# Performance work log

Hardware: AMD Instinct MI355X
Metric: run time of the kernel (lower is better)

## Reference

```python
import jax, jax.numpy as jnp
import numpy as np

D = 768
H = 12
DH = D // H
PAIRS4 = [(0, 1), (0, 2), (0, 3), (1, 2), (1, 3), (2, 3)]
J6 = jnp.array([[0,0,0,0,0,1],[0,0,0,0,-1,0],[0,0,0,1,0,0],[0,0,1,0,0,0],[0,-1,0,0,0,0],[1,0,0,0,0,0]], dtype=jnp.float32)


def exterior(p1, p2):
    # p1,p2: (..., 4) -> normalized Plucker coords (..., 6)
    parts = [p1[..., i] * p2[..., j] - p1[..., j] * p2[..., i] for i, j in PAIRS4]
    L = jnp.stack(parts, axis=-1)
    n = jnp.clip(jnp.linalg.norm(L, axis=-1, keepdims=True), 1e-12)
    return L / n


def layernorm(x, g, b, eps=1e-5):
    m = jnp.mean(x, axis=-1, keepdims=True)
    v = jnp.var(x, axis=-1, keepdims=True)
    return (x - m) * jax.lax.rsqrt(v + eps) * g + b


def setup_inputs() -> dict:
    key = jax.random.key(0)
    ks = jax.random.split(key, 16)
    s = 0.02
    inp = {
        'x': jax.random.normal(ks[0], (1, 2048, D), dtype=jnp.float32),
        'ln1_g': jnp.ones((D,), jnp.float32), 'ln1_b': jnp.zeros((D,), jnp.float32),
        'qkv_w': jax.random.normal(ks[1], (D, 3 * D), jnp.float32) * s,
        'qkv_b': jnp.zeros((3 * D,), jnp.float32),
        'w1_write': jax.random.normal(ks[2], (D, 4 * H), jnp.float32) * s,
        'w2_write': jax.random.normal(ks[3], (D, 4 * H), jnp.float32) * s,
        'w1_read': jax.random.normal(ks[4], (D, 4 * H), jnp.float32) * s,
        'w2_read': jax.random.normal(ks[5], (D, 4 * H), jnp.float32) * s,
        'geo_v_w': jax.random.normal(ks[6], (D, D), jnp.float32) * s,
        'geo_v_b': jnp.zeros((D,), jnp.float32),
        'gate_w': jax.random.normal(ks[7], (D, H), jnp.float32) * s,
        'gate_b': jnp.zeros((H,), jnp.float32),
        'inc_scale': jnp.ones((H,), jnp.float32),
        'out_w': jax.random.normal(ks[8], (D, D), jnp.float32) * s,
        'out_b': jnp.zeros((D,), jnp.float32),
        'ln2_g': jnp.ones((D,), jnp.float32), 'ln2_b': jnp.zeros((D,), jnp.float32),
        'fc_w': jax.random.normal(ks[9], (D, 4 * D), jnp.float32) * s,
        'fc_b': jnp.zeros((4 * D,), jnp.float32),
        'proj_w': jax.random.normal(ks[10], (4 * D, D), jnp.float32) * s,
        'proj_b': jnp.zeros((D,), jnp.float32),
    }
    return inp


def dual_path_attention(x, qkv_w, qkv_b, w1_write, w2_write, w1_read, w2_read,
                        geo_v_w, geo_v_b, gate_w, gate_b, inc_scale, out_w, out_b):
    B, T, _ = x.shape
    scale = DH ** -0.5
    qkv = (x @ qkv_w + qkv_b).reshape(B, T, 3, H, DH)
    q = qkv[:, :, 0].transpose(0, 2, 1, 3)  # (B,H,T,dh)
    k = qkv[:, :, 1].transpose(0, 2, 1, 3)
    v = qkv[:, :, 2].transpose(0, 2, 1, 3)
    std_logits = jnp.einsum('bhtd,bhsd->bhts', q, k) * scale

    x_prev = jnp.concatenate([jnp.zeros((B, 1, x.shape[-1]), x.dtype), x[:, :-1]], axis=1)
    w1 = (x_prev @ w1_write).reshape(B, T, H, 4)
    w2 = (x @ w2_write).reshape(B, T, H, 4)
    write_lines = exterior(w1, w2)  # (B,T,H,6)
    r1 = (x @ w1_read).reshape(B, T, H, 4)
    r2 = (x @ w2_read).reshape(B, T, H, 4)
    read_lines = exterior(r1, r2)
    J_write = jnp.einsum('bthi,ij->bthj', write_lines, J6)
    geo_logits = jnp.einsum('bthp,bshp->bhts', read_lines, J_write)
    geo_logits = geo_logits * inc_scale[None, :, None, None]

    mask = jnp.triu(jnp.ones((T, T), dtype=bool), k=1)  # True above diagonal
    neg = jnp.finfo(x.dtype).min
    std_attn = jax.nn.softmax(jnp.where(mask, neg, std_logits), axis=-1)
    std_out = jnp.einsum('bhts,bhsd->bthd', std_attn, v).reshape(B, T, -1)
    geo_attn = jax.nn.softmax(jnp.where(mask, neg, geo_logits), axis=-1)
    geo_v = (x @ geo_v_w + geo_v_b).reshape(B, T, H, DH).transpose(0, 2, 1, 3)
    geo_out = jnp.einsum('bhts,bhsd->bthd', geo_attn, geo_v).reshape(B, T, -1)

    gate = jax.nn.sigmoid(x @ gate_w + gate_b).mean(axis=-1, keepdims=True)
    combined = (1 - gate) * std_out + gate * geo_out
    return combined @ out_w + out_b


def reference(x, ln1_g, ln1_b, qkv_w, qkv_b, w1_write, w2_write, w1_read, w2_read,
              geo_v_w, geo_v_b, gate_w, gate_b, inc_scale, out_w, out_b,
              ln2_g, ln2_b, fc_w, fc_b, proj_w, proj_b):
    h = x + dual_path_attention(layernorm(x, ln1_g, ln1_b), qkv_w, qkv_b,
                                w1_write, w2_write, w1_read, w2_read,
                                geo_v_w, geo_v_b, gate_w, gate_b, inc_scale,
                                out_w, out_b)
    m = layernorm(h, ln2_g, ln2_b)
    mlp = jax.nn.gelu(m @ fc_w + fc_b) @ proj_w + proj_b
    return h + mlp
```

## Files before the change

### kernel.cpp

```cpp
#include <hip/hip_runtime.h>
#include <hip/hip_bf16.h>
#include <math.h>

#define TT 2048
#define DD 768

typedef __bf16 bf16x8 __attribute__((ext_vector_type(8)));
typedef float f32x4 __attribute__((ext_vector_type(4)));

__device__ __forceinline__ void gload16(const void* g, void* l) {
    __builtin_amdgcn_global_load_lds(
        (const __attribute__((address_space(1))) unsigned int*)g,
        (__attribute__((address_space(3))) unsigned int*)l, 16, 0, 0);
}

__device__ __forceinline__ bf16x8 zero8() {
    bf16x8 v;
    #pragma unroll
    for (int j = 0; j < 8; ++j) v[j] = (__bf16)0.0f;
    return v;
}

__global__ __launch_bounds__(256) void ln_kernel(const float* __restrict__ in,
    const float* __restrict__ g, const float* __restrict__ b,
    __hip_bfloat16* __restrict__ out)
{
    const int t = blockIdx.x;
    const int tid = threadIdx.x;
    const float* row = in + (size_t)t * DD;
    float x0 = row[tid], x1 = row[tid + 256], x2 = row[tid + 512];
    float s = x0 + x1 + x2;
    float q = x0 * x0 + x1 * x1 + x2 * x2;
    #pragma unroll
    for (int m = 1; m < 64; m <<= 1) {
        s += __shfl_xor(s, m);
        q += __shfl_xor(q, m);
    }
    __shared__ float ssum[4], sqsum[4];
    const int w = tid >> 6;
    if ((tid & 63) == 0) { ssum[w] = s; sqsum[w] = q; }
    __syncthreads();
    s = ssum[0] + ssum[1] + ssum[2] + ssum[3];
    q = sqsum[0] + sqsum[1] + sqsum[2] + sqsum[3];
    const float mean = s * (1.0f / DD);
    const float var = q * (1.0f / DD) - mean * mean;
    const float rs = rsqrtf(var + 1e-5f);
    __hip_bfloat16* orow = out + (size_t)t * DD;
    orow[tid]       = __float2bfloat16((x0 - mean) * rs * g[tid]       + b[tid]);
    orow[tid + 256] = __float2bfloat16((x1 - mean) * rs * g[tid + 256] + b[tid + 256]);
    orow[tid + 512] = __float2bfloat16((x2 - mean) * rs * g[tid + 512] + b[tid + 512]);
}

__global__ __launch_bounds__(256) void castT_kernel(const float* __restrict__ in,
    __hip_bfloat16* __restrict__ out, int K, int N)
{
    __shared__ float t[32][33];
    const int n0 = blockIdx.x << 5, k0 = blockIdx.y << 5;
    const int tx = threadIdx.x & 31, ty = threadIdx.x >> 5;
    #pragma unroll
    for (int i = 0; i < 32; i += 8)
        t[ty + i][tx] = in[(size_t)(k0 + ty + i) * N + n0 + tx];
    __syncthreads();
    #pragma unroll
    for (int i = 0; i < 32; i += 8)
        out[(size_t)(n0 + ty + i) * K + k0 + tx] = __float2bfloat16(t[tx][ty + i]);
}

__global__ __launch_bounds__(256) void wcat_kernel(
    const float* __restrict__ w2w, const float* __restrict__ w1w,
    const float* __restrict__ w1r, const float* __restrict__ w2r,
    const float* __restrict__ gw, __hip_bfloat16* __restrict__ Wcat)
{
    const int nrow = blockIdx.x;
    const float* src; int col, stride;
    if (nrow < 48)       { src = w2w; col = nrow;       stride = 48; }
    else if (nrow < 96)  { src = w1w; col = nrow - 48;  stride = 48; }
    else if (nrow < 144) { src = w1r; col = nrow - 96;  stride = 48; }
    else if (nrow < 192) { src = w2r; col = nrow - 144; stride = 48; }
    else                 { src = gw;  col = nrow - 192; stride = 12; }
    const int tid = threadIdx.x;
    #pragma unroll
    for (int i = 0; i < 3; ++i) {
        const int k = tid + (i << 8);
        Wcat[(size_t)nrow * 768 + k] = __float2bfloat16(src[(size_t)k * stride + col]);
    }
}

__device__ __forceinline__ float gelu_f(float x) {
    float u = 0.7978845608028654f * (x + 0.044715f * x * x * x);
    return 0.5f * x * (1.0f + tanhf(u));
}

__global__ __launch_bounds__(256) void mgemm64_kernel(
    const __hip_bfloat16* __restrict__ A, const __hip_bfloat16* __restrict__ Bt,
    const float* __restrict__ bias, const float* __restrict__ resid,
    void* __restrict__ Cout, float* __restrict__ Pb0, float* __restrict__ Pb1,
    int M, int N, int K, int kz, int epi, int omode)
{
    __shared__ __hip_bfloat16 As[64 * 32];
    __shared__ __hip_bfloat16 Bs[128 * 32];
    const int tid = threadIdx.x;
    const int lane = tid & 63, w = tid >> 6;
    const int colBase = blockIdx.x << 7, rowBase = blockIdx.y << 6;
    const int z = blockIdx.z;
    const int Kc = K / kz, koff = z * Kc;

    const int lr = lane >> 2, pc = lane & 3;
    const int n = lane & 15, quad = lane >> 4;

    const int arow = (w << 4) + lr;
    const int ac = (pc ^ ((arow >> 1) & 3)) << 3;
    const int brow0 = (w << 5) + lr, brow1 = brow0 + 16;
    const int bc0 = (pc ^ ((brow0 >> 1) & 3)) << 3;
    const int bc1 = (pc ^ ((brow1 >> 1) & 3)) << 3;

    f32x4 acc[8];
    #pragma unroll
    for (int j = 0; j < 8; ++j) acc[j] = (f32x4){0.f, 0.f, 0.f, 0.f};

    const int arF = (w << 4) + n;
    const int aposF = (quad ^ ((arF >> 1) & 3)) << 3;

    for (int kk = koff; kk < koff + Kc; kk += 32) {
        __syncthreads();
        gload16(A  + (size_t)(rowBase + arow) * K + kk + ac,   &As[(w << 4) * 32]);
        gload16(Bt + (size_t)(colBase + brow0) * K + kk + bc0, &Bs[(w << 5) * 32]);
        gload16(Bt + (size_t)(colBase + brow1) * K + kk + bc1, &Bs[((w << 5) + 16) * 32]);
        __syncthreads();

        bf16x8 af = *(const bf16x8*)&As[arF * 32 + aposF];
        #pragma unroll
        for (int j = 0; j < 8; ++j) {
            const int rb = (j << 4) + n;
            bf16x8 bfj = *(const bf16x8*)&Bs[rb * 32 + ((quad ^ ((rb >> 1) & 3)) << 3)];
            acc[j] = __builtin_amdgcn_mfma_f32_16x16x32_bf16(af, bfj, acc[j], 0, 0, 0);
        }
    }

    if (kz == 1) {
        #pragma unroll
        for (int j = 0; j < 8; ++j) {
            const int col = colBase + (j << 4) + n;
            const float bj = bias ? bias[col] : 0.f;
            #pragma unroll
            for (int r = 0; r < 4; ++r) {
                const int row = rowBase + (w << 4) + (quad << 2) + r;
                float v = acc[j][r] + bj;
                if (epi == 1) v = gelu_f(v);
                else if (epi == 2) v += resid[(size_t)row * N + col];
                if (omode == 1) ((__hip_bfloat16*)Cout)[(size_t)row * N + col] = __float2bfloat16(v);
                else ((float*)Cout)[(size_t)row * N + col] = v;
            }
        }
    } else {
        float* P = (z == 0) ? Pb0 : Pb1;
        #pragma unroll
        for (int j = 0; j < 8; ++j) {
            const int col = colBase + (j << 4) + n;
            #pragma unroll
            for (int r = 0; r < 4; ++r) {
                const int row = rowBase + (w << 4) + (quad << 2) + r;
                P[(size_t)row * N + col] = acc[j][r];
            }
        }
    }
}

__global__ __launch_bounds__(256) void kred_kernel(
    const float* __restrict__ p0, const float* __restrict__ p1,
    const float* __restrict__ bias, const float* __restrict__ resid,
    float* __restrict__ out, int N)
{
    const int base = (blockIdx.x * 256 + threadIdx.x) << 2;
    float4 a = *(const float4*)&p0[base];
    float4 b = *(const float4*)&p1[base];
    float4 bi = *(const float4*)&bias[base % N];
    float4 rs = *(const float4*)&resid[base];
    float4 o;
    o.x = a.x + b.x + bi.x + rs.x;
    o.y = a.y + b.y + bi.y + rs.y;
    o.z = a.z + b.z + bi.z + rs.z;
    o.w = a.w + b.w + bi.w + rs.w;
    *(float4*)&out[base] = o;
}

__device__ __forceinline__ void exterior6(const float* a, const float* b, float* L) {
    L[0] = a[0] * b[1] - a[1] * b[0];
    L[1] = a[0] * b[2] - a[2] * b[0];
    L[2] = a[0] * b[3] - a[3] * b[0];
    L[3] = a[1] * b[2] - a[2] * b[1];
    L[4] = a[1] * b[3] - a[3] * b[1];
    L[5] = a[2] * b[3] - a[3] * b[2];
    float n = sqrtf(L[0]*L[0] + L[1]*L[1] + L[2]*L[2] + L[3]*L[3] + L[4]*L[4] + L[5]*L[5]);
    float inv = 1.f / fmaxf(n, 1e-12f);
    #pragma unroll
    for (int p = 0; p < 6; ++p) L[p] *= inv;
}

__global__ __launch_bounds__(64) void extgate_kernel(
    const float* __restrict__ P, const float* __restrict__ gb,
    __hip_bfloat16* __restrict__ rlb, __hip_bfloat16* __restrict__ jwb,
    float* __restrict__ gate)
{
    const int t = blockIdx.x;
    const int tid = threadIdx.x;
    const float* row = P + (size_t)t * 256;
    if (tid < 12) {
        const int h = tid;
        float a[4], b[4], L[6];
        #pragma unroll
        for (int i = 0; i < 4; ++i) {
            a[i] = (t > 0) ? row[-256 + 48 + h * 4 + i] : 0.f;
            b[i] = row[h * 4 + i];
        }
        exterior6(a, b, L);
        __hip_bfloat16* jwp = jwb + (size_t)h * 16384 + t * 8;
        jwp[0] = __float2bfloat16( L[5]); jwp[1] = __float2bfloat16(-L[4]);
        jwp[2] = __float2bfloat16( L[3]); jwp[3] = __float2bfloat16( L[2]);
        jwp[4] = __float2bfloat16(-L[1]); jwp[5] = __float2bfloat16( L[0]);
        jwp[6] = __float2bfloat16(0.f);   jwp[7] = __float2bfloat16(0.f);
        #pragma unroll
        for (int i = 0; i < 4; ++i) { a[i] = row[96 + h * 4 + i]; b[i] = row[144 + h * 4 + i]; }
        exterior6(a, b, L);
        __hip_bfloat16* rlp = rlb + (size_t)h * 16384 + t * 8;
        #pragma unroll
        for (int p = 0; p < 6; ++p) rlp[p] = __float2bfloat16(L[p]);
        rlp[6] = __float2bfloat16(0.f); rlp[7] = __float2bfloat16(0.f);
    }
    if (tid == 32) {
        float g = 0.f;
        #pragma unroll
        for (int i = 0; i < 12; ++i) g += 1.f / (1.f + __expf(-(row[192 + i] + gb[i])));
        gate[t] = g * (1.f / 12.f);
    }
}

__global__ __launch_bounds__(256) void vt_kernel(
    const __hip_bfloat16* __restrict__ qkvB, const __hip_bfloat16* __restrict__ geovB,
    __hip_bfloat16* __restrict__ VT, __hip_bfloat16* __restrict__ GVT)
{
    __shared__ __hip_bfloat16 tile[64][72];
    const int s0 = blockIdx.x << 6, h = blockIdx.y;
    const bool isGV = (blockIdx.z != 0);
    const __hip_bfloat16* src = isGV ? (geovB + h * 64) : (qkvB + 1536 + h * 64);
    const int stride = isGV ? 768 : 2304;
    __hip_bfloat16* dst = (isGV ? GVT : VT) + (size_t)h * 131072;
    const int tid = threadIdx.x;
    const int r = tid >> 2, c = (tid & 3) << 3;
    *(bf16x8*)&tile[r][c]      = *(const bf16x8*)&src[(size_t)(s0 + r) * stride + c];
    *(bf16x8*)&tile[r][c + 32] = *(const bf16x8*)&src[(size_t)(s0 + r) * stride + c + 32];
    __syncthreads();
    __hip_bfloat16 tmp[8];
    #pragma unroll
    for (int j = 0; j < 8; ++j) tmp[j] = tile[c + j][r];
    *(bf16x8*)&dst[(size_t)r * 2048 + s0 + c] = *(const bf16x8*)tmp;
    #pragma unroll
    for (int j = 0; j < 8; ++j) tmp[j] = tile[c + 32 + j][r];
    *(bf16x8*)&dst[(size_t)r * 2048 + s0 + c + 32] = *(const bf16x8*)tmp;
}

__global__ __launch_bounds__(256) void mattn_kernel(
    const __hip_bfloat16* __restrict__ qkvB, const __hip_bfloat16* __restrict__ VT,
    const __hip_bfloat16* __restrict__ GVT, const __hip_bfloat16* __restrict__ rlb,
    const __hip_bfloat16* __restrict__ jwb, const float* __restrict__ gate,
    const float* __restrict__ inc_scale, __hip_bfloat16* __restrict__ comb,
    __hip_bfloat16* __restrict__ Opart, float* __restrict__ stats)
{
    __shared__ __hip_bfloat16 Ks0[2048], Ks1[2048];
    __shared__ __hip_bfloat16 VTs0[2048], VTs1[2048];
    __shared__ __hip_bfloat16 GVTs0[2048], GVTs1[2048];
    __shared__ __hip_bfloat16 JWs[64][8];
    __shared__ __bf16 Ps[64][72];
    __shared__ __bf16 Pg[64][72];

    const int j = 59 - blockIdx.x;
    const int hh = blockIdx.y;
    int qt, c, nc;
    if (j < 12)      { qt = j; c = 0; nc = 1; }
    else if (j < 36) { int t2 = j - 12; qt = 12 + (t2 >> 1); c = t2 & 1; nc = 2; }
    else             { int t2 = j - 36; int d3 = t2 / 3; qt = 24 + d3; c = t2 - d3 * 3; nc = 3; }
    const int q0 = qt << 6;
    const int nk = qt + 1;
    const int ktb = c * nk / nc;
    const int kte = (c + 1) * nk / nc - 1;
    const int tid = threadIdx.x;
    const int w = tid >> 6, lane = tid & 63;
    const int n = lane & 15, quad = lane >> 4;

    const int qrow = q0 + (w << 4) + n;
    const size_t qb = (size_t)qrow * 2304 + hh * 64;
    bf16x8 af0 = *(const bf16x8*)&qkvB[qb + (quad << 3)];
    bf16x8 af1 = *(const bf16x8*)&qkvB[qb + 32 + (quad << 3)];
    bf16x8 rlA = zero8();
    if (quad == 0) rlA = *(const bf16x8*)&rlb[(size_t)hh * 16384 + (size_t)qrow * 8];
    const float isc = inc_scale[hh];
    const float mgc = fabsf(isc);
    const size_t vbase = (size_t)hh * 131072;

    const int sRow = tid >> 2, sc = tid & 3;
    const int sPos = ((sc ^ ((sRow >> 1) & 3)) << 3);
    const int sOff = sc << 3;

    f32x4 Os[4], Og[4];
    float m_s[4], lsp[4], lgp[4];
    #pragma unroll
    for (int r = 0; r < 4; ++r) {
        m_s[r] = -1e30f; lsp[r] = 0.f; lgp[r] = 0.f;
        Os[r] = (f32x4){0.f, 0.f, 0.f, 0.f};
        Og[r] = (f32x4){0.f, 0.f, 0.f, 0.f};
    }

    bf16x8 rK0, rK1, rV0, rV1, rG0, rG1, rJ = zero8();
    {
        const int k0 = ktb << 6;
        const size_t kb = (size_t)(k0 + sRow) * 2304 + 768 + hh * 64;
        const size_t vb = vbase + (size_t)sRow * 2048 + k0;
        rK0 = *(const bf16x8*)&qkvB[kb + sOff];
        rK1 = *(const bf16x8*)&qkvB[kb + sOff + 32];
        rV0 = *(const bf16x8*)&VT[vb + sOff];
        rV1 = *(const bf16x8*)&VT[vb + sOff + 32];
        rG0 = *(const bf16x8*)&GVT[vb + sOff];
        rG1 = *(const bf16x8*)&GVT[vb + sOff + 32];
        if (tid < 64) rJ = *(const bf16x8*)&jwb[(size_t)hh * 16384 + (size_t)(k0 + tid) * 8];
    }

    for (int kt = ktb; kt <= kte; ++kt) {
        const int k0 = kt << 6;
        __syncthreads();
        *(bf16x8*)&Ks0[sRow * 32 + sPos]  = rK0;
        *(bf16x8*)&Ks1[sRow * 32 + sPos]  = rK1;
        *(bf16x8*)&VTs0[sRow * 32 + sPos] = rV0;
        *(bf16x8*)&VTs1[sRow * 32 + sPos] = rV1;
        *(bf16x8*)&GVTs0[sRow * 32 + sPos] = rG0;
        *(bf16x8*)&GVTs1[sRow * 32 + sPos] = rG1;
        if (tid < 64) *(bf16x8*)&JWs[tid][0] = rJ;
        if (kt < kte) {
            const int k1 = (kt + 1) << 6;
            const size_t kb = (size_t)(k1 + sRow) * 2304 + 768 + hh * 64;
            const size_t vb = vbase + (size_t)sRow * 2048 + k1;
            rK0 = *(const bf16x8*)&qkvB[kb + sOff];
            rK1 = *(const bf16x8*)&qkvB[kb + sOff + 32];
            rV0 = *(const bf16x8*)&VT[vb + sOff];
            rV1 = *(const bf16x8*)&VT[vb + sOff + 32];
            rG0 = *(const bf16x8*)&GVT[vb + sOff];
            rG1 = *(const bf16x8*)&GVT[vb + sOff + 32];
            if (tid < 64) rJ = *(const bf16x8*)&jwb[(size_t)hh * 16384 + (size_t)(k1 + tid) * 8];
        }
        __syncthreads();

        f32x4 Ss[4], Sg[4];
        #pragma unroll
        for (int t = 0; t < 4; ++t) {
            Ss[t] = (f32x4){0.f, 0.f, 0.f, 0.f};
            Sg[t] = (f32x4){0.f, 0.f, 0.f, 0.f};
        }
        #pragma unroll
        for (int t = 0; t < 4; ++t) {
            const int krow = (t << 4) + n;
            const int kpos = ((quad ^ ((krow >> 1) & 3)) << 3);
            bf16x8 kb0 = *(const bf16x8*)&Ks0[krow * 32 + kpos];
            bf16x8 kb1 = *(const bf16x8*)&Ks1[krow * 32 + kpos];
            Ss[t] = __builtin_amdgcn_mfma_f32_16x16x32_bf16(af0, kb0, Ss[t], 0, 0, 0);
            Ss[t] = __builtin_amdgcn_mfma_f32_16x16x32_bf16(af1, kb1, Ss[t], 0, 0, 0);
            bf16x8 jb = zero8();
            if (quad == 0) jb = *(const bf16x8*)&JWs[krow][0];
            Sg[t] = __builtin_amdgcn_mfma_f32_16x16x32_bf16(rlA, jb, Sg[t], 0, 0, 0);
        }
        #pragma unroll
        for (int t = 0; t < 4; ++t) {
            #pragma unroll
            for (int r = 0; r < 4; ++r) { Ss[t][r] *= 0.125f; Sg[t][r] *= isc; }
        }
        if (kt == qt) {
            #pragma unroll
            for (int t = 0; t < 4; ++t) {
                const int sg = k0 + (t << 4) + n;
                #pragma unroll
                for (int r = 0; r < 4; ++r) {
                    const int qg = q0 + (w << 4) + (quad << 2) + r;
                    if (sg > qg) { Ss[t][r] = -1e30f; Sg[t][r] = -1e30f; }
                }
            }
        }

        #pragma unroll
        for (int r = 0; r < 4; ++r) {
            float mx = fmaxf(fmaxf(Ss[0][r], Ss[1][r]), fmaxf(Ss[2][r], Ss[3][r]));
            #pragma unroll
            for (int mk = 1; mk < 16; mk <<= 1) mx = fmaxf(mx, __shfl_xor(mx, mk));
            float mnew = fmaxf(m_s[r], mx);
            float alpha = __expf(m_s[r] - mnew);
            m_s[r] = mnew;
            float sm = 0.f;
            #pragma unroll
            for (int t = 0; t < 4; ++t) { Ss[t][r] = __expf(Ss[t][r] - mnew); sm += Ss[t][r]; }
            lsp[r] = lsp[r] * alpha + sm;
            #pragma unroll
            for (int t = 0; t < 4; ++t) Os[t][r] *= alpha;

            float smg = 0.f;
            #pragma unroll
            for (int t = 0; t < 4; ++t) { Sg[t][r] = __expf(Sg[t][r] - mgc); smg += Sg[t][r]; }
            lgp[r] += smg;
        }

        #pragma unroll
        for (int t = 0; t < 4; ++t) {
            #pragma unroll
            for (int r = 0; r < 4; ++r) {
                Ps[(w << 4) + (quad << 2) + r][(t << 4) + n] = (__bf16)Ss[t][r];
                Pg[(w << 4) + (quad << 2) + r][(t << 4) + n] = (__bf16)Sg[t][r];
            }
        }
        asm volatile("s_waitcnt lgkmcnt(0)" ::: "memory");

        #pragma unroll
        for (int st = 0; st < 2; ++st) {
            bf16x8 ap = *(const bf16x8*)&Ps[(w << 4) + n][(st << 5) + (quad << 3)];
            bf16x8 gp = *(const bf16x8*)&Pg[(w << 4) + n][(st << 5) + (quad << 3)];
            const __hip_bfloat16* Vh = st ? VTs1 : VTs0;
            const __hip_bfloat16* Gh = st ? GVTs1 : GVTs0;
            #pragma unroll
            for (int dt = 0; dt < 4; ++dt) {
                const int vrow = (dt << 4) + n;
                const int vpos = ((quad ^ ((vrow >> 1) & 3)) << 3);
                bf16x8 vb2 = *(const bf16x8*)&Vh[vrow * 32 + vpos];
                bf16x8 gb2 = *(const bf16x8*)&Gh[vrow * 32 + vpos];
                Os[dt] = __builtin_amdgcn_mfma_f32_16x16x32_bf16(ap, vb2, Os[dt], 0, 0, 0);
                Og[dt] = __builtin_amdgcn_mfma_f32_16x16x32_bf16(gp, gb2, Og[dt], 0, 0, 0);
            }
        }
    }

    float l_s[4], l_g[4];
    #pragma unroll
    for (int r = 0; r < 4; ++r) {
        float ls = lsp[r], lg = lgp[r];
        #pragma unroll
        for (int mk = 1; mk < 16; mk <<= 1) {
            ls += __shfl_xor(ls, mk);
            lg += __shfl_xor(lg, mk);
        }
        l_s[r] = ls; l_g[r] = lg;
    }

    if (nc == 1) {
        #pragma unroll
        for (int r = 0; r < 4; ++r) {
            const int row = q0 + (w << 4) + (quad << 2) + r;
            const float g = gate[row];
            const float invs = (1.f - g) / l_s[r], invg = g / l_g[r];
            #pragma unroll
            for (int dt = 0; dt < 4; ++dt) {
                float val = Os[dt][r] * invs + Og[dt][r] * invg;
                comb[(size_t)row * DD + hh * 64 + (dt << 4) + n] = __float2bfloat16(val);
            }
        }
    } else {
        const int base = (qt < 24) ? ((qt - 12) << 1) : (24 + (qt - 24) * 3);
        const int slot = hh * 48 + base + c;
        __hip_bfloat16* op = Opart + (size_t)slot * 8192;
        float* st = stats + (size_t)slot * 256;
        #pragma unroll
        for (int r = 0; r < 4; ++r) {
            const int rloc = (w << 4) + (quad << 2) + r;
            #pragma unroll
            for (int dt = 0; dt < 4; ++dt) {
                const int col = (dt << 4) + n;
                op[rloc * 128 + col]      = __float2bfloat16(Os[dt][r]);
                op[rloc * 128 + 64 + col] = __float2bfloat16(Og[dt][r]);
            }
            if (n == 0) {
                st[rloc * 4 + 0] = m_s[r]; st[rloc * 4 + 1] = l_s[r];
                st[rloc * 4 + 2] = mgc;    st[rloc * 4 + 3] = l_g[r];
            }
        }
    }
}

__global__ __launch_bounds__(256) void acomb_kernel(
    const __hip_bfloat16* __restrict__ Opart, const float* __restrict__ stats,
    const float* __restrict__ gate, __hip_bfloat16* __restrict__ comb)
{
    const int qt = 12 + blockIdx.x;
    const int h = blockIdx.y;
    const int nc = (qt < 24) ? 2 : 3;
    const int sb = h * 48 + ((qt < 24) ? ((qt - 12) << 1) : (24 + (qt - 24) * 3));
    const int tid = threadIdx.x;
    const int rloc = tid >> 2;
    const int cseg = (tid & 3) << 4;
    const int row = (qt << 6) + rloc;
    float ms = -1e30f, mg = -1e30f;
    for (int c = 0; c < nc; ++c) {
        const float* st = stats + (size_t)(sb + c) * 256 + rloc * 4;
        ms = fmaxf(ms, st[0]);
        mg = fmaxf(mg, st[2]);
    }
    float wsc[3], wgc[3];
    float ls = 0.f, lg = 0.f;
    for (int c = 0; c < nc; ++c) {
        const float* st = stats + (size_t)(sb + c) * 256 + rloc * 4;
        wsc[c] = __expf(st[0] - ms); ls += st[1] * wsc[c];
        wgc[c] = __expf(st[2] - mg); lg += st[3] * wgc[c];
    }
    const float g = gate[row];
    const float fs = (1.f - g) / ls, fg = g / lg;
    #pragma unroll
    for (int cc = 0; cc < 16; ++cc) {
        const int col = cseg + cc;
        float os = 0.f, og = 0.f;
        for (int c = 0; c < nc; ++c) {
            const __hip_bfloat16* op = Opart + (size_t)(sb + c) * 8192 + rloc * 128;
            os += __bfloat162float(op[col]) * wsc[c];
            og += __bfloat162float(op[64 + col]) * wgc[c];
        }
        comb[(size_t)row * DD + h * 64 + col] = __float2bfloat16(os * fs + og * fg);
    }
}

extern "C" void kernel_launch(void* const* d_in, const int* in_sizes, int n_in,
                              void* d_out, int out_size, void* d_ws, size_t ws_size,
                              hipStream_t stream) {
    (void)in_sizes; (void)n_in; (void)out_size; (void)ws_size;
    const float* x      = (const float*)d_in[0];
    const float* ln1_g  = (const float*)d_in[1];
    const float* ln1_b  = (const float*)d_in[2];
    const float* qkv_w  = (const float*)d_in[3];
    const float* qkv_b  = (const float*)d_in[4];
    const float* w1w    = (const float*)d_in[5];
    const float* w2w    = (const float*)d_in[6];
    const float* w1r    = (const float*)d_in[7];
    const float* w2r    = (const float*)d_in[8];
    const float* gvw    = (const float*)d_in[9];
    const float* gvb    = (const float*)d_in[10];
    const float* gw     = (const float*)d_in[11];
    const float* gb     = (const float*)d_in[12];
    const float* isc    = (const float*)d_in[13];
    const float* ow     = (const float*)d_in[14];
    const float* ob     = (const float*)d_in[15];
    const float* ln2_g  = (const float*)d_in[16];
    const float* ln2_b  = (const float*)d_in[17];
    const float* fcw    = (const float*)d_in[18];
    const float* fcb    = (const float*)d_in[19];
    const float* pw     = (const float*)d_in[20];
    const float* pb     = (const float*)d_in[21];
    float* out = (float*)d_out;
    char* wsb  = (char*)d_ws;

    __hip_bfloat16* qkvB  = (__hip_bfloat16*)(wsb + 0);
    __hip_bfloat16* geovB = (__hip_bfloat16*)(wsb + 9437184);
    __hip_bfloat16* VTb   = (__hip_bfloat16*)(wsb + 12582912);
    __hip_bfloat16* GVTb  = (__hip_bfloat16*)(wsb + 15728640);
    __hip_bfloat16* rlb   = (__hip_bfloat16*)(wsb + 18874368);
    __hip_bfloat16* jwb   = (__hip_bfloat16*)(wsb + 19267584);
    float*          gate  = (float*)(wsb + 19660800);
    __hip_bfloat16* ln1   = (__hip_bfloat16*)(wsb + 19668992);
    __hip_bfloat16* comb  = (__hip_bfloat16*)(wsb + 22814720);
    float*          hbuf  = (float*)(wsb + 25960448);
    __hip_bfloat16* qkvwt = (__hip_bfloat16*)(wsb + 32251904);
    __hip_bfloat16* gvwt  = (__hip_bfloat16*)(wsb + 35790848);
    __hip_bfloat16* owt   = (__hip_bfloat16*)(wsb + 36970496);
    float*          stats = (float*)(wsb + 38150144);
    __hip_bfloat16* Opart = (__hip_bfloat16*)hbuf;
    __hip_bfloat16* fcwt  = qkvwt;
    __hip_bfloat16* pwt   = (__hip_bfloat16*)(wsb + 0);
    __hip_bfloat16* fcact = (__hip_bfloat16*)(wsb + 4718592);
    float* Ppart0 = (float*)(wsb + 18874368);
    float* Ppart1 = (float*)(wsb + 32251904);
    __hip_bfloat16* Wcat  = owt;
    float*          Pproj = (float*)(wsb + 22814720);

    castT_kernel<<<dim3(72, 24), 256, 0, stream>>>(qkv_w, qkvwt, 768, 2304);
    castT_kernel<<<dim3(24, 24), 256, 0, stream>>>(gvw, gvwt, 768, 768);
    wcat_kernel<<<204, 256, 0, stream>>>(w2w, w1w, w1r, w2r, gw, Wcat);
    ln_kernel<<<TT, 256, 0, stream>>>(x, ln1_g, ln1_b, ln1);
    mgemm64_kernel<<<dim3(2, 32, 1), 256, 0, stream>>>(ln1, Wcat, nullptr, nullptr, Pproj, nullptr, nullptr, TT, 256, 768, 1, 0, 0);
    extgate_kernel<<<TT, 64, 0, stream>>>(Pproj, gb, rlb, jwb, gate);
    mgemm64_kernel<<<dim3(18, 32, 1), 256, 0, stream>>>(ln1, qkvwt, qkv_b, nullptr, qkvB, nullptr, nullptr, TT, 2304, 768, 1, 0, 1);
    mgemm64_kernel<<<dim3(6, 32, 1), 256, 0, stream>>>(ln1, gvwt, gvb, nullptr, geovB, nullptr, nullptr, TT, 768, 768, 1, 0, 1);
    vt_kernel<<<dim3(32, 12, 2), 256, 0, stream>>>(qkvB, geovB, VTb, GVTb);
    mattn_kernel<<<dim3(60, 12), 256, 0, stream>>>(qkvB, VTb, GVTb, rlb, jwb, gate, isc, comb, Opart, stats);
    acomb_kernel<<<dim3(20, 12), 256, 0, stream>>>(Opart, stats, gate, comb);
    castT_kernel<<<dim3(24, 24), 256, 0, stream>>>(ow, owt, 768, 768);
    mgemm64_kernel<<<dim3(6, 32, 1), 256, 0, stream>>>(comb, owt, ob, x, hbuf, nullptr, nullptr, TT, 768, 768, 1, 2, 0);
    ln_kernel<<<TT, 256, 0, stream>>>(hbuf, ln2_g, ln2_b, ln1);
    castT_kernel<<<dim3(96, 24), 256, 0, stream>>>(fcw, fcwt, 768, 3072);
    mgemm64_kernel<<<dim3(24, 32, 1), 256, 0, stream>>>(ln1, fcwt, fcb, nullptr, fcact, nullptr, nullptr, TT, 3072, 768, 1, 1, 1);
    castT_kernel<<<dim3(24, 96), 256, 0, stream>>>(pw, pwt, 3072, 768);
    mgemm64_kernel<<<dim3(6, 32, 2), 256, 0, stream>>>(fcact, pwt, pb, nullptr, nullptr, Ppart0, Ppart1, TT, 768, 3072, 2, 0, 0);
    kred_kernel<<<1536, 256, 0, stream>>>(Ppart0, Ppart1, pb, hbuf, out, 768);
}
```

Before: 357.0 us.

## Fuse QKV, geo-V and projection GEMMs into one wide GEMM; rebalance attention splits

Concatenates the QKV, geo-value and small projection/gate weights into one 3328-column bf16 weight matrix so a single GEMM produces all of them, replacing three launches. The projection outputs now arrive in bf16 rather than fp32 before the exterior-product step, which costs some precision. The attention kernel gets a new key-split schedule (one more chunk every 9 query tiles, 74 blocks per head) and a launch_bounds occupancy hint. It also reuses one shared P buffer for the standard and geometric paths to cut LDS use. Partial outputs are spread across three aliased workspace regions.

```diff
diff --git a/kernel.cpp b/kernel.cpp
--- a/kernel.cpp
+++ b/kernel.cpp
@@ -19,6 +19,14 @@
     #pragma unroll
     for (int j = 0; j < 8; ++j) v[j] = (__bf16)0.0f;
     return v;
+}
+
+__device__ __forceinline__ const __hip_bfloat16* opart_cptr(
+    const __hip_bfloat16* pA, const __hip_bfloat16* pB, const __hip_bfloat16* pC, int slot)
+{
+    if (slot < 192) return pA + (size_t)slot * 8192;
+    if (slot < 576) return pB + (size_t)(slot - 192) * 8192;
+    return pC + (size_t)(slot - 576) * 8192;
 }
 
 __global__ __launch_bounds__(256) void ln_kernel(const float* __restrict__ in,
@@ -69,20 +77,28 @@
 __global__ __launch_bounds__(256) void wcat_kernel(
     const float* __restrict__ w2w, const float* __restrict__ w1w,
     const float* __restrict__ w1r, const float* __restrict__ w2r,
-    const float* __restrict__ gw, __hip_bfloat16* __restrict__ Wcat)
-{
-    const int nrow = blockIdx.x;
+    const float* __restrict__ gw, const float* __restrict__ qkv_b,
+    const float* __restrict__ gvb, __hip_bfloat16* __restrict__ Wcat,
+    float* __restrict__ bias3)
+{
+    const int bid = blockIdx.x;
+    const int tid = threadIdx.x;
+    if (bid >= 204) {
+        const int idx = (bid - 204) * 256 + tid;
+        float v = (idx < 2304) ? qkv_b[idx] : ((idx < 3072) ? gvb[idx - 2304] : 0.f);
+        bias3[idx] = v;
+        return;
+    }
     const float* src; int col, stride;
-    if (nrow < 48)       { src = w2w; col = nrow;       stride = 48; }
-    else if (nrow < 96)  { src = w1w; col = nrow - 48;  stride = 48; }
-    else if (nrow < 144) { src = w1r; col = nrow - 96;  stride = 48; }
-    else if (nrow < 192) { src = w2r; col = nrow - 144; stride = 48; }
-    else                 { src = gw;  col = nrow - 192; stride = 12; }
-    const int tid = threadIdx.x;
+    if (bid < 48)       { src = w2w; col = bid;       stride = 48; }
+    else if (bid < 96)  { src = w1w; col = bid - 48;  stride = 48; }
+    else if (bid < 144) { src = w1r; col = bid - 96;  stride = 48; }
+    else if (bid < 192) { src = w2r; col = bid - 144; stride = 48; }
+    else                { src = gw;  col = bid - 192; stride = 12; }
     #pragma unroll
     for (int i = 0; i < 3; ++i) {
         const int k = tid + (i << 8);
-        Wcat[(size_t)nrow * 768 + k] = __float2bfloat16(src[(size_t)k * stride + col]);
+        Wcat[(size_t)bid * 768 + k] = __float2bfloat16(src[(size_t)k * stride + col]);
     }
 }
 
@@ -198,20 +214,20 @@
 }
 
 __global__ __launch_bounds__(64) void extgate_kernel(
-    const float* __restrict__ P, const float* __restrict__ gb,
+    const __hip_bfloat16* __restrict__ Pall, const float* __restrict__ gb,
     __hip_bfloat16* __restrict__ rlb, __hip_bfloat16* __restrict__ jwb,
     float* __restrict__ gate)
 {
     const int t = blockIdx.x;
     const int tid = threadIdx.x;
-    const float* row = P + (size_t)t * 256;
+    const __hip_bfloat16* row = Pall + (size_t)t * 3328 + 3072;
     if (tid < 12) {
         const int h = tid;
         float a[4], b[4], L[6];
         #pragma unroll
         for (int i = 0; i < 4; ++i) {
-            a[i] = (t > 0) ? row[-256 + 48 + h * 4 + i] : 0.f;
-            b[i] = row[h * 4 + i];
+            a[i] = (t > 0) ? __bfloat162float(row[-3328 + 48 + h * 4 + i]) : 0.f;
+            b[i] = __bfloat162float(row[h * 4 + i]);
         }
         exterior6(a, b, L);
         __hip_bfloat16* jwp = jwb + (size_t)h * 16384 + t * 8;
@@ -220,7 +236,10 @@
         jwp[4] = __float2bfloat16(-L[1]); jwp[5] = __float2bfloat16( L[0]);
         jwp[6] = __float2bfloat16(0.f);   jwp[7] = __float2bfloat16(0.f);
         #pragma unroll
-        for (int i = 0; i < 4; ++i) { a[i] = row[96 + h * 4 + i]; b[i] = row[144 + h * 4 + i]; }
+        for (int i = 0; i < 4; ++i) {
+            a[i] = __bfloat162float(row[96 + h * 4 + i]);
+            b[i] = __bfloat162float(row[144 + h * 4 + i]);
+        }
         exterior6(a, b, L);
         __hip_bfloat16* rlp = rlb + (size_t)h * 16384 + t * 8;
         #pragma unroll
@@ -230,25 +249,25 @@
     if (tid == 32) {
         float g = 0.f;
         #pragma unroll
-        for (int i = 0; i < 12; ++i) g += 1.f / (1.f + __expf(-(row[192 + i] + gb[i])));
+        for (int i = 0; i < 12; ++i)
+            g += 1.f / (1.f + __expf(-(__bfloat162float(row[192 + i]) + gb[i])));
         gate[t] = g * (1.f / 12.f);
     }
 }
 
 __global__ __launch_bounds__(256) void vt_kernel(
-    const __hip_bfloat16* __restrict__ qkvB, const __hip_bfloat16* __restrict__ geovB,
+    const __hip_bfloat16* __restrict__ qkvAll,
     __hip_bfloat16* __restrict__ VT, __hip_bfloat16* __restrict__ GVT)
 {
     __shared__ __hip_bfloat16 tile[64][72];
     const int s0 = blockIdx.x << 6, h = blockIdx.y;
     const bool isGV = (blockIdx.z != 0);
-    const __hip_bfloat16* src = isGV ? (geovB + h * 64) : (qkvB + 1536 + h * 64);
-    const int stride = isGV ? 768 : 2304;
+    const __hip_bfloat16* src = qkvAll + (isGV ? 2304 : 1536) + h * 64;
     __hip_bfloat16* dst = (isGV ? GVT : VT) + (size_t)h * 131072;
     const int tid = threadIdx.x;
     const int r = tid >> 2, c = (tid & 3) << 3;
-    *(bf16x8*)&tile[r][c]      = *(const bf16x8*)&src[(size_t)(s0 + r) * stride + c];
-    *(bf16x8*)&tile[r][c + 32] = *(const bf16x8*)&src[(size_t)(s0 + r) * stride + c + 32];
+    *(bf16x8*)&tile[r][c]      = *(const bf16x8*)&src[(size_t)(s0 + r) * 3328 + c];
+    *(bf16x8*)&tile[r][c + 32] = *(const bf16x8*)&src[(size_t)(s0 + r) * 3328 + c + 32];
     __syncthreads();
     __hip_bfloat16 tmp[8];
     #pragma unroll
@@ -259,26 +278,30 @@
     *(bf16x8*)&dst[(size_t)r * 2048 + s0 + c + 32] = *(const bf16x8*)tmp;
 }
 
-__global__ __launch_bounds__(256) void mattn_kernel(
-    const __hip_bfloat16* __restrict__ qkvB, const __hip_bfloat16* __restrict__ VT,
+__global__ __launch_bounds__(256, 4) void mattn_kernel(
+    const __hip_bfloat16* __restrict__ qkvAll, const __hip_bfloat16* __restrict__ VT,
     const __hip_bfloat16* __restrict__ GVT, const __hip_bfloat16* __restrict__ rlb,
     const __hip_bfloat16* __restrict__ jwb, const float* __restrict__ gate,
     const float* __restrict__ inc_scale, __hip_bfloat16* __restrict__ comb,
-    __hip_bfloat16* __restrict__ Opart, float* __restrict__ stats)
+    __hip_bfloat16* __restrict__ OpA, __hip_bfloat16* __restrict__ OpB,
+    __hip_bfloat16* __restrict__ OpC, float* __restrict__ stats)
 {
     __shared__ __hip_bfloat16 Ks0[2048], Ks1[2048];
     __shared__ __hip_bfloat16 VTs0[2048], VTs1[2048];
     __shared__ __hip_bfloat16 GVTs0[2048], GVTs1[2048];
     __shared__ __hip_bfloat16 JWs[64][8];
     __shared__ __bf16 Ps[64][72];
-    __shared__ __bf16 Pg[64][72];
-
-    const int j = 59 - blockIdx.x;
+
+    const int j = blockIdx.x;
     const int hh = blockIdx.y;
-    int qt, c, nc;
-    if (j < 12)      { qt = j; c = 0; nc = 1; }
-    else if (j < 36) { int t2 = j - 12; qt = 12 + (t2 >> 1); c = t2 & 1; nc = 2; }
-    else             { int t2 = j - 36; int d3 = t2 / 3; qt = 24 + d3; c = t2 - d3 * 3; nc = 3; }
+    int qt = 0, acc = 0, nc = 1;
+    #pragma unroll 1
+    for (;;) {
+        nc = (qt + 9) / 9;
+        if (j < acc + nc) break;
+        acc += nc; ++qt;
+    }
+    const int c = j - acc;
     const int q0 = qt << 6;
     const int nk = qt + 1;
     const int ktb = c * nk / nc;
@@ -288,9 +311,9 @@
     const int n = lane & 15, quad = lane >> 4;
 
     const int qrow = q0 + (w << 4) + n;
-    const size_t qb = (size_t)qrow * 2304 + hh * 64;
-    bf16x8 af0 = *(const bf16x8*)&qkvB[qb + (quad << 3)];
-    bf16x8 af1 = *(const bf16x8*)&qkvB[qb + 32 + (quad << 3)];
+    const size_t qb = (size_t)qrow * 3328 + hh * 64;
+    bf16x8 af0 = *(const bf16x8*)&qkvAll[qb + (quad << 3)];
+    bf16x8 af1 = *(const bf16x8*)&qkvAll[qb + 32 + (quad << 3)];
     bf16x8 rlA = zero8();
     if (quad == 0) rlA = *(const bf16x8*)&rlb[(size_t)hh * 16384 + (size_t)qrow * 8];
     const float isc = inc_scale[hh];
@@ -313,10 +336,10 @@
     bf16x8 rK0, rK1, rV0, rV1, rG0, rG1, rJ = zero8();
     {
         const int k0 = ktb << 6;
-        const size_t kb = (size_t)(k0 + sRow) * 2304 + 768 + hh * 64;
+        const size_t kb = (size_t)(k0 + sRow) * 3328 + 768 + hh * 64;
         const size_t vb = vbase + (size_t)sRow * 2048 + k0;
-        rK0 = *(const bf16x8*)&qkvB[kb + sOff];
-        rK1 = *(const bf16x8*)&qkvB[kb + sOff + 32];
+        rK0 = *(const bf16x8*)&qkvAll[kb + sOff];
+        rK1 = *(const bf16x8*)&qkvAll[kb + sOff + 32];
         rV0 = *(const bf16x8*)&VT[vb + sOff];
         rV1 = *(const bf16x8*)&VT[vb + sOff + 32];
         rG0 = *(const bf16x8*)&GVT[vb + sOff];
@@ -336,10 +359,10 @@
         if (tid < 64) *(bf16x8*)&JWs[tid][0] = rJ;
         if (kt < kte) {
             const int k1 = (kt + 1) << 6;
-            const size_t kb = (size_t)(k1 + sRow) * 2304 + 768 + hh * 64;
+            const size_t kb = (size_t)(k1 + sRow) * 3328 + 768 + hh * 64;
             const size_t vb = vbase + (size_t)sRow * 2048 + k1;
-            rK0 = *(const bf16x8*)&qkvB[kb + sOff];
-            rK1 = *(const bf16x8*)&qkvB[kb + sOff + 32];
+            rK0 = *(const bf16x8*)&qkvAll[kb + sOff];
+            rK1 = *(const bf16x8*)&qkvAll[kb + sOff + 32];
             rV0 = *(const bf16x8*)&VT[vb + sOff];
             rV1 = *(const bf16x8*)&VT[vb + sOff + 32];
             rG0 = *(const bf16x8*)&GVT[vb + sOff];
@@ -407,26 +430,40 @@
         #pragma unroll
         for (int t = 0; t < 4; ++t) {
             #pragma unroll
-            for (int r = 0; r < 4; ++r) {
+            for (int r = 0; r < 4; ++r)
                 Ps[(w << 4) + (quad << 2) + r][(t << 4) + n] = (__bf16)Ss[t][r];
-                Pg[(w << 4) + (quad << 2) + r][(t << 4) + n] = (__bf16)Sg[t][r];
-            }
         }
         asm volatile("s_waitcnt lgkmcnt(0)" ::: "memory");
-
         #pragma unroll
         for (int st = 0; st < 2; ++st) {
             bf16x8 ap = *(const bf16x8*)&Ps[(w << 4) + n][(st << 5) + (quad << 3)];
-            bf16x8 gp = *(const bf16x8*)&Pg[(w << 4) + n][(st << 5) + (quad << 3)];
             const __hip_bfloat16* Vh = st ? VTs1 : VTs0;
-            const __hip_bfloat16* Gh = st ? GVTs1 : GVTs0;
             #pragma unroll
             for (int dt = 0; dt < 4; ++dt) {
                 const int vrow = (dt << 4) + n;
                 const int vpos = ((quad ^ ((vrow >> 1) & 3)) << 3);
                 bf16x8 vb2 = *(const bf16x8*)&Vh[vrow * 32 + vpos];
+                Os[dt] = __builtin_amdgcn_mfma_f32_16x16x32_bf16(ap, vb2, Os[dt], 0, 0, 0);
+            }
+        }
+        asm volatile("s_waitcnt lgkmcnt(0)" ::: "memory");
+
+        #pragma unroll
+        for (int t = 0; t < 4; ++t) {
+            #pragma unroll
+            for (int r = 0; r < 4; ++r)
+                Ps[(w << 4) + (quad << 2) + r][(t << 4) + n] = (__bf16)Sg[t][r];
+        }
+        asm volatile("s_waitcnt lgkmcnt(0)" ::: "memory");
+        #pragma unroll
+        for (int st = 0; st < 2; ++st) {
+            bf16x8 gp = *(const bf16x8*)&Ps[(w << 4) + n][(st << 5) + (quad << 3)];
+            const __hip_bfloat16* Gh = st ? GVTs1 : GVTs0;
+            #pragma unroll
+            for (int dt = 0; dt < 4; ++dt) {
+                const int vrow = (dt << 4) + n;
+                const int vpos = ((quad ^ ((vrow >> 1) & 3)) << 3);
                 bf16x8 gb2 = *(const bf16x8*)&Gh[vrow * 32 + vpos];
-                Os[dt] = __builtin_amdgcn_mfma_f32_16x16x32_bf16(ap, vb2, Os[dt], 0, 0, 0);
                 Og[dt] = __builtin_amdgcn_mfma_f32_16x16x32_bf16(gp, gb2, Og[dt], 0, 0, 0);
             }
         }
@@ -457,9 +494,8 @@
             }
         }
     } else {
-        const int base = (qt < 24) ? ((qt - 12) << 1) : (24 + (qt - 24) * 3);
-        const int slot = hh * 48 + base + c;
-        __hip_bfloat16* op = Opart + (size_t)slot * 8192;
+        const int slot = hh * 74 + acc + c;
+        __hip_bfloat16* op = (__hip_bfloat16*)opart_cptr(OpA, OpB, OpC, slot);
         float* st = stats + (size_t)slot * 256;
         #pragma unroll
         for (int r = 0; r < 4; ++r) {
@@ -479,13 +515,17 @@
 }
 
 __global__ __launch_bounds__(256) void acomb_kernel(
-    const __hip_bfloat16* __restrict__ Opart, const float* __restrict__ stats,
+    const __hip_bfloat16* __restrict__ OpA, const __hip_bfloat16* __restrict__ OpB,
+    const __hip_bfloat16* __restrict__ OpC, const float* __restrict__ stats,
     const float* __restrict__ gate, __hip_bfloat16* __restrict__ comb)
 {
-    const int qt = 12 + blockIdx.x;
+    const int qt = 9 + blockIdx.x;
     const int h = blockIdx.y;
-    const int nc = (qt < 24) ? 2 : 3;
-    const int sb = h * 48 + ((qt < 24) ? ((qt - 12) << 1) : (24 + (qt - 24) * 3));
+    const int nc = (qt + 9) / 9;
+    int acc = 0;
+    #pragma unroll 1
+    for (int q = 0; q < qt; ++q) acc += (q + 9) / 9;
+    const int sb = h * 74 + acc;
     const int tid = threadIdx.x;
     const int rloc = tid >> 2;
     const int cseg = (tid & 3) << 4;
@@ -496,7 +536,7 @@
         ms = fmaxf(ms, st[0]);
         mg = fmaxf(mg, st[2]);
     }
-    float wsc[3], wgc[3];
+    float wsc[4], wgc[4];
     float ls = 0.f, lg = 0.f;
     for (int c = 0; c < nc; ++c) {
         const float* st = stats + (size_t)(sb + c) * 256 + rloc * 4;
@@ -510,7 +550,7 @@
         const int col = cseg + cc;
         float os = 0.f, og = 0.f;
         for (int c = 0; c < nc; ++c) {
-            const __hip_bfloat16* op = Opart + (size_t)(sb + c) * 8192 + rloc * 128;
+            const __hip_bfloat16* op = opart_cptr(OpA, OpB, OpC, sb + c) + rloc * 128;
             os += __bfloat162float(op[col]) * wsc[c];
             og += __bfloat162float(op[64 + col]) * wgc[c];
         }
@@ -547,46 +587,51 @@
     float* out = (float*)d_out;
     char* wsb  = (char*)d_ws;
 
-    __hip_bfloat16* qkvB  = (__hip_bfloat16*)(wsb + 0);
-    __hip_bfloat16* geovB = (__hip_bfloat16*)(wsb + 9437184);
-    __hip_bfloat16* VTb   = (__hip_bfloat16*)(wsb + 12582912);
-    __hip_bfloat16* GVTb  = (__hip_bfloat16*)(wsb + 15728640);
-    __hip_bfloat16* rlb   = (__hip_bfloat16*)(wsb + 18874368);
-    __hip_bfloat16* jwb   = (__hip_bfloat16*)(wsb + 19267584);
-    float*          gate  = (float*)(wsb + 19660800);
-    __hip_bfloat16* ln1   = (__hip_bfloat16*)(wsb + 19668992);
-    __hip_bfloat16* comb  = (__hip_bfloat16*)(wsb + 22814720);
-    float*          hbuf  = (float*)(wsb + 25960448);
-    __hip_bfloat16* qkvwt = (__hip_bfloat16*)(wsb + 32251904);
-    __hip_bfloat16* gvwt  = (__hip_bfloat16*)(wsb + 35790848);
-    __hip_bfloat16* owt   = (__hip_bfloat16*)(wsb + 36970496);
-    float*          stats = (float*)(wsb + 38150144);
-    __hip_bfloat16* Opart = (__hip_bfloat16*)hbuf;
-    __hip_bfloat16* fcwt  = qkvwt;
-    __hip_bfloat16* pwt   = (__hip_bfloat16*)(wsb + 0);
-    __hip_bfloat16* fcact = (__hip_bfloat16*)(wsb + 4718592);
-    float* Ppart0 = (float*)(wsb + 18874368);
-    float* Ppart1 = (float*)(wsb + 32251904);
-    __hip_bfloat16* Wcat  = owt;
-    float*          Pproj = (float*)(wsb + 22814720);
-
-    castT_kernel<<<dim3(72, 24), 256, 0, stream>>>(qkv_w, qkvwt, 768, 2304);
-    castT_kernel<<<dim3(24, 24), 256, 0, stream>>>(gvw, gvwt, 768, 768);
-    wcat_kernel<<<204, 256, 0, stream>>>(w2w, w1w, w1r, w2r, gw, Wcat);
+    __hip_bfloat16* qkvAll = (__hip_bfloat16*)(wsb + 0);
+    __hip_bfloat16* VTb    = (__hip_bfloat16*)(wsb + 13631488);
+    __hip_bfloat16* GVTb   = (__hip_bfloat16*)(wsb + 16777216);
+    __hip_bfloat16* rlb    = (__hip_bfloat16*)(wsb + 19922944);
+    __hip_bfloat16* jwb    = (__hip_bfloat16*)(wsb + 20316160);
+    float*          gate   = (float*)(wsb + 20709376);
+    __hip_bfloat16* ln1    = (__hip_bfloat16*)(wsb + 20717568);
+    __hip_bfloat16* comb   = (__hip_bfloat16*)(wsb + 23863296);
+    float*          hbuf   = (float*)(wsb + 27009024);
+    __hip_bfloat16* Bt     = (__hip_bfloat16*)(wsb + 33300480);
+    float*          bias3  = (float*)(wsb + 38412288);
+    __hip_bfloat16* owt    = (__hip_bfloat16*)(wsb + 38425600);
+
+    __hip_bfloat16* OpA   = ln1;
+    __hip_bfloat16* OpB   = (__hip_bfloat16*)hbuf;
+    __hip_bfloat16* OpC   = Bt;
+    float*          stats = (float*)owt;
+
+    __hip_bfloat16* fcact  = qkvAll;
+    __hip_bfloat16* pwt    = VTb;
+    __hip_bfloat16* fcwt   = Bt;
+    float* Ppart0 = (float*)(wsb + 20717568);
+    float* Ppart1 = (float*)(wsb + 33300480);
+
+    castT_kernel<<<dim3(72, 24), 256, 0, stream>>>(qkv_w, Bt, 768, 2304);
+    castT_kernel<<<dim3(24, 24), 256, 0, stream>>>(gvw, Bt + (size_t)2304 * 768, 768, 768);
+    wcat_kernel<<<217, 256, 0, stream>>>(w2w, w1w, w1r, w2r, gw, qkv_b, gvb,
+                                         Bt + (size_t)3072 * 768, bias3);
     ln_kernel<<<TT, 256, 0, stream>>>(x, ln1_g, ln1_b, ln1);
-    mgemm64_kernel<<<dim3(2, 32, 1), 256, 0, stream>>>(ln1, Wcat, nullptr, nullptr, Pproj, nullptr, nullptr, TT, 256, 768, 1, 0, 0);
-    extgate_kernel<<<TT, 64, 0, stream>>>(Pproj, gb, rlb, jwb, gate);
-    mgemm64_kernel<<<dim3(18, 32, 1), 256, 0, stream>>>(ln1, qkvwt, qkv_b, nullptr, qkvB, nullptr, nullptr, TT, 2304, 768, 1, 0, 1);
-    mgemm64_kernel<<<dim3(6, 32, 1), 256, 0, stream>>>(ln1, gvwt, gvb, nullptr, geovB, nullptr, nullptr, TT, 768, 768, 1, 0, 1);
-    vt_kernel<<<dim3(32, 12, 2), 256, 0, stream>>>(qkvB, geovB, VTb, GVTb);
-    mattn_kernel<<<dim3(60, 12), 256, 0, stream>>>(qkvB, VTb, GVTb, rlb, jwb, gate, isc, comb, Opart, stats);
-    acomb_kernel<<<dim3(20, 12), 256, 0, stream>>>(Opart, stats, gate, comb);
+    mgemm64_kernel<<<dim3(26, 32, 1), 256, 0, stream>>>(ln1, Bt, bias3, nullptr, qkvAll,
+                                                        nullptr, nullptr, TT, 3328, 768, 1, 0, 1);
+    extgate_kernel<<<TT, 64, 0, stream>>>(qkvAll, gb, rlb, jwb, gate);
+    vt_kernel<<<dim3(32, 12, 2), 256, 0, stream>>>(qkvAll, VTb, GVTb);
+    mattn_kernel<<<dim3(74, 12), 256, 0, stream>>>(qkvAll, VTb, GVTb, rlb, jwb, gate, isc,
+                                                   comb, OpA, OpB, OpC, stats);
+    acomb_kernel<<<dim3(23, 12), 256, 0, stream>>>(OpA, OpB, OpC, stats, gate, comb);
     castT_kernel<<<dim3(24, 24), 256, 0, stream>>>(ow, owt, 768, 768);
-    mgemm64_kernel<<<dim3(6, 32, 1), 256, 0, stream>>>(comb, owt, ob, x, hbuf, nullptr, nullptr, TT, 768, 768, 1, 2, 0);
+    mgemm64_kernel<<<dim3(6, 32, 1), 256, 0, stream>>>(comb, owt, ob, x, hbuf,
+                                                       nullptr, nullptr, TT, 768, 768, 1, 2, 0);
     ln_kernel<<<TT, 256, 0, stream>>>(hbuf, ln2_g, ln2_b, ln1);
     castT_kernel<<<dim3(96, 24), 256, 0, stream>>>(fcw, fcwt, 768, 3072);
-    mgemm64_kernel<<<dim3(24, 32, 1), 256, 0, stream>>>(ln1, fcwt, fcb, nullptr, fcact, nullptr, nullptr, TT, 3072, 768, 1, 1, 1);
+    mgemm64_kernel<<<dim3(24, 32, 1), 256, 0, stream>>>(ln1, fcwt, fcb, nullptr, fcact,
+                                                        nullptr, nullptr, TT, 3072, 768, 1, 1, 1);
     castT_kernel<<<dim3(24, 96), 256, 0, stream>>>(pw, pwt, 3072, 768);
-    mgemm64_kernel<<<dim3(6, 32, 2), 256, 0, stream>>>(fcact, pwt, pb, nullptr, nullptr, Ppart0, Ppart1, TT, 768, 3072, 2, 0, 0);
+    mgemm64_kernel<<<dim3(6, 32, 2), 256, 0, stream>>>(fcact, pwt, pb, nullptr, nullptr,
+                                                       Ppart0, Ppart1, TT, 768, 3072, 2, 0, 0);
     kred_kernel<<<1536, 256, 0, stream>>>(Ppart0, Ppart1, pb, hbuf, out, 768);
 }
```

New measurement: 395.8 us. 10.9% more time.
